# Optimization experiments

Hardware: AMD Instinct MI355X
Metric: run time of the kernel (lower is better)

The kernel has to match this reference:

```python
import jax, jax.numpy as jnp
import numpy as np
from jax import lax

N_LEVELS = 16
N_NODES = 65536  # nodes per level (= batch_size of trees at the root level)
FEATURES = 7
HIDDEN = 64


def setup_inputs() -> dict:
    key = jax.random.key(0)
    ks = jax.random.split(key, 11)
    contents = jax.random.normal(ks[0], (N_LEVELS, N_NODES, FEATURES), dtype=jnp.float32)
    children = jax.random.randint(ks[1], (N_LEVELS - 1, N_NODES, 2), 0, N_NODES, dtype=jnp.int32)
    s = 0.05
    return {
        'contents': contents,
        'children': children,
        'Wu': jax.random.normal(ks[2], (HIDDEN, FEATURES), dtype=jnp.float32) * s,
        'bu': jax.random.normal(ks[3], (HIDDEN,), dtype=jnp.float32) * s,
        'Wr': jax.random.normal(ks[4], (3 * HIDDEN, 3 * HIDDEN), dtype=jnp.float32) * s,
        'br': jax.random.normal(ks[5], (3 * HIDDEN,), dtype=jnp.float32) * s,
        'Wh': jax.random.normal(ks[6], (HIDDEN, 3 * HIDDEN), dtype=jnp.float32) * s,
        'bh': jax.random.normal(ks[7], (HIDDEN,), dtype=jnp.float32) * s,
        'Wz': jax.random.normal(ks[8], (4 * HIDDEN, 4 * HIDDEN), dtype=jnp.float32) * s,
        'bz': jax.random.normal(ks[9], (4 * HIDDEN,), dtype=jnp.float32) * s,
    }


def reference(contents, children, Wu, bu, Wr, br, Wh, bh, Wz, bz):
    h = Wu.shape[0]

    def leaf_embed(c):  # fc_u + relu
        return jax.nn.relu(c @ Wu.T + bu)

    # deepest level: all leaves -> up_embedding is just u_k
    up_top = leaf_embed(contents[-1])

    def step(up_next, xs):
        c, ch = xs                      # c: [N,F], ch: [N,2]
        u_k = leaf_embed(c)             # [N,h]
        h_L = up_next[ch[:, 0]]         # gather left children  [N,h]
        h_R = up_next[ch[:, 1]]         # gather right children [N,h]
        hhu = jnp.concatenate([h_L, h_R, u_k], axis=1)          # [N,3h]
        r = jax.nn.sigmoid(hhu @ Wr.T + br)                     # fc_r gate
        h_H = jax.nn.relu((r * hhu) @ Wh.T + bh)                # fc_h
        z = jnp.concatenate([h_H, hhu], axis=-1) @ Wz.T + bz    # [N,4h]
        # torch.stack([z_H,z_L,z_R,z_N],2) -> [N,h,4]; softmax over dim=1 (hidden)
        z = jnp.transpose(z.reshape(-1, 4, h), (0, 2, 1))       # [N,h,4]
        z = jax.nn.softmax(z, axis=1)
        h_new = z[:, :, 0] * h_H + z[:, :, 1] * h_L + z[:, :, 2] * h_R + z[:, :, 3] * u_k
        return h_new, None

    # process levels n-2, ..., 0 (bottom-up)
    xs = (contents[:-1][::-1], children[::-1])
    up0, _ = lax.scan(step, up_top, xs)
    # level 0 has batch_size roots -> h_out shape [batch_size, hidden]
    return up0
```

## Files before the change

### kernel.cpp

```cpp
#include <hip/hip_runtime.h>
#include <math.h>


#define N_NODES 65536
#define FEAT 7
#define H 64
#define MT 32
#define BLK 256

typedef __attribute__((ext_vector_type(8))) short bf16x8;
typedef __attribute__((ext_vector_type(4))) short short4v;
typedef __attribute__((ext_vector_type(4))) float f32x4;

__device__ __forceinline__ void split_bf16(float x, short& hi, short& lo) {
    unsigned u = __float_as_uint(x);
    unsigned r = (u + 0x7fffu + ((u >> 16) & 1u)) >> 16;
    hi = (short)r;
    float res = x - __uint_as_float(r << 16);
    unsigned u2 = __float_as_uint(res);
    unsigned r2 = (u2 + 0x7fffu + ((u2 >> 16) & 1u)) >> 16;
    lo = (short)r2;
}
__device__ __forceinline__ float bf2f(short h) {
    return __uint_as_float(((unsigned)(unsigned short)h) << 16);
}
__device__ __forceinline__ int zbidx(int row, int col) {
    return row * 192 + ((((col >> 3) ^ (row & 7)) << 3) | (col & 7));
}
__device__ __forceinline__ int zaidx(int row, int col) {
    return row * 64 + ((((col >> 3) ^ (row & 7)) << 3) | (col & 7));
}

#define MFMA3(acc, ah, al, bh8, bl8)                                              \
    acc = __builtin_amdgcn_mfma_f32_16x16x32_bf16(al, bh8, acc, 0, 0, 0);         \
    acc = __builtin_amdgcn_mfma_f32_16x16x32_bf16(ah, bl8, acc, 0, 0, 0);         \
    acc = __builtin_amdgcn_mfma_f32_16x16x32_bf16(ah, bh8, acc, 0, 0, 0);

__global__ __launch_bounds__(256) void grnn_prep(
    const float* __restrict__ Wr, const float* __restrict__ Wh,
    const float* __restrict__ Wz, short* __restrict__ wsp)
{
    int job = blockIdx.x * 4 + (threadIdx.x >> 6);
    int lane = threadIdx.x & 63;
    const float* src; int K, t, s; short* dst;
    short* ws_wh = wsp + 72 * 1024;
    short* ws_wz = wsp + 96 * 1024;
    if (job < 72)       { t = job / 6;            s = job % 6;        K = 192; src = Wr; dst = wsp   + job * 1024; }
    else if (job < 96)  { int j = job - 72; t = j / 6; s = j % 6;     K = 192; src = Wh; dst = ws_wh + j * 1024; }
    else                { int j = job - 96; t = j / 8; s = j % 8;     K = 256; src = Wz; dst = ws_wz + j * 1024; }
    int i  = t * 16 + (lane & 15);
    int k0 = s * 32 + (lane >> 4) * 8;
    const float* p = src + (size_t)i * K + k0;
    bf16x8 hi, lo;
#pragma unroll
    for (int e = 0; e < 8; ++e) { short h, l; split_bf16(p[e], h, l); hi[e] = h; lo[e] = l; }
    *(bf16x8*)(dst + lane * 8) = hi;
    *(bf16x8*)(dst + 512 + lane * 8) = lo;
}

__global__ __launch_bounds__(BLK) void grnn_leaf_kernel(
    const float* __restrict__ contents, const float* __restrict__ Wu,
    const float* __restrict__ bu, float* __restrict__ h_out)
{
    int t = blockIdx.x * BLK + threadIdx.x;
    int node = t >> 6;
    int j = t & 63;
    const float* c = contents + (size_t)15 * N_NODES * FEAT + (size_t)node * FEAT;
    float acc = bu[j];
#pragma unroll
    for (int f = 0; f < FEAT; ++f) acc += c[f] * Wu[j * FEAT + f];
    h_out[t] = fmaxf(acc, 0.f);
}

__global__ __launch_bounds__(BLK) void grnn_step_mfma(
    const float* __restrict__ contents_k, const int* __restrict__ children_k,
    const float* __restrict__ h_in,
    const float* __restrict__ Wu, const float* __restrict__ bu,
    const float* __restrict__ br, const float* __restrict__ bh,
    const float* __restrict__ bz,
    const short* __restrict__ wsp, float* __restrict__ h_out)
{
    __shared__ __align__(16) short zb_hi[MT * 192];
    __shared__ __align__(16) short zb_lo[MT * 192];
    __shared__ __align__(16) short ubuf[2][MT * 192];
    __shared__ __align__(16) float hacc[MT * 68];

    const int tid = threadIdx.x;
    const int node0 = blockIdx.x * MT;
    const int wv = tid >> 6, lane = tid & 63, lr = lane & 15, lh = lane >> 4;
    const short* wr_s = wsp;
    const short* wh_s = wsp + 72 * 1024;
    const short* wz_s = wsp + 96 * 1024;
    const f32x4 z4 = {0.f, 0.f, 0.f, 0.f};

    {
        int row = tid >> 2, q = tid & 3;
        int nd = row >> 1, side = row & 1;
        int child = children_k[(size_t)(node0 + nd) * 2 + side];
        const float4* src = (const float4*)(h_in + (size_t)child * H + q * 16);
#pragma unroll
        for (int f = 0; f < 4; ++f) {
            float4 v = src[f];
            float vv[4] = {v.x, v.y, v.z, v.w};
            int col0 = side * 64 + q * 16 + f * 4;
            int idx = zbidx(nd, col0);
            short4v h4, l4;
#pragma unroll
            for (int e = 0; e < 4; ++e) {
                short h, l; split_bf16(vv[e], h, l);
                h4[e] = h; l4[e] = l;
            }
            *(short4v*)&zb_hi[idx] = h4;
            *(short4v*)&zb_lo[idx] = l4;
        }
    }
    {
        int nd = tid >> 3, j0 = (tid & 7) * 8;
        float c[FEAT];
#pragma unroll
        for (int f = 0; f < FEAT; ++f) c[f] = contents_k[(size_t)(node0 + nd) * FEAT + f];
        bf16x8 hv, lv;
#pragma unroll
        for (int jj = 0; jj < 8; ++jj) {
            int j = j0 + jj;
            float a = bu[j];
#pragma unroll
            for (int f = 0; f < FEAT; ++f) a += c[f] * Wu[j * FEAT + f];
            a = fmaxf(a, 0.f);
            short h, l; split_bf16(a, h, l); hv[jj] = h; lv[jj] = l;
        }
        int idx = zbidx(nd, 128 + j0);
        *(bf16x8*)&zb_hi[idx] = hv;
        *(bf16x8*)&zb_lo[idx] = lv;
    }
    __syncthreads();

    f32x4 acc1[2][3];
#pragma unroll
    for (int mi = 0; mi < 2; ++mi)
#pragma unroll
        for (int ni = 0; ni < 3; ++ni) acc1[mi][ni] = z4;
    for (int s = 0; s < 6; ++s) {
        bf16x8 ah[2], al[2];
#pragma unroll
        for (int mi = 0; mi < 2; ++mi) {
            int idx = zbidx(mi * 16 + lr, s * 32 + lh * 8);
            ah[mi] = *(const bf16x8*)&zb_hi[idx];
            al[mi] = *(const bf16x8*)&zb_lo[idx];
        }
#pragma unroll
        for (int ni = 0; ni < 3; ++ni) {
            const short* bp = wr_s + ((3 * wv + ni) * 6 + s) * 1024;
            bf16x8 bh8 = *(const bf16x8*)(bp + lane * 8);
            bf16x8 bl8 = *(const bf16x8*)(bp + 512 + lane * 8);
#pragma unroll
            for (int mi = 0; mi < 2; ++mi) { MFMA3(acc1[mi][ni], ah[mi], al[mi], bh8, bl8); }
        }
    }
#pragma unroll
    for (int ni = 0; ni < 3; ++ni) {
        int i = (3 * wv + ni) * 16 + lr;
        float brv = br[i];
#pragma unroll
        for (int mi = 0; mi < 2; ++mi) {
#pragma unroll
            for (int r = 0; r < 4; ++r) {
                int nd = mi * 16 + lh * 4 + r;
                float v = acc1[mi][ni][r] + brv;
                float sg = 1.f / (1.f + __expf(-v));
                int xi = zbidx(nd, i);
                float x = bf2f(zb_hi[xi]) + bf2f(zb_lo[xi]);
                short h, l; split_bf16(sg * x, h, l);
                ubuf[0][xi] = h;
                ubuf[1][xi] = l;
            }
        }
    }
    __syncthreads();

    f32x4 acc2[2] = {z4, z4};
    for (int s = 0; s < 6; ++s) {
        bf16x8 ah[2], al[2];
#pragma unroll
        for (int mi = 0; mi < 2; ++mi) {
            int idx = zbidx(mi * 16 + lr, s * 32 + lh * 8);
            ah[mi] = *(const bf16x8*)&ubuf[0][idx];
            al[mi] = *(const bf16x8*)&ubuf[1][idx];
        }
        const short* bp = wh_s + (wv * 6 + s) * 1024;
        bf16x8 bh8 = *(const bf16x8*)(bp + lane * 8);
        bf16x8 bl8 = *(const bf16x8*)(bp + 512 + lane * 8);
#pragma unroll
        for (int mi = 0; mi < 2; ++mi) { MFMA3(acc2[mi], ah[mi], al[mi], bh8, bl8); }
    }
    __syncthreads();
    {
        int j = wv * 16 + lr;
        float bhv = bh[j];
#pragma unroll
        for (int mi = 0; mi < 2; ++mi) {
#pragma unroll
            for (int r = 0; r < 4; ++r) {
                int nd = mi * 16 + lh * 4 + r;
                float v = fmaxf(acc2[mi][r] + bhv, 0.f);
                short h, l; split_bf16(v, h, l);
                int idx = zaidx(nd, j);
                ubuf[0][idx] = h;
                ubuf[1][idx] = l;
            }
        }
    }
    __syncthreads();

    f32x4 acc3[2][4];
#pragma unroll
    for (int mi = 0; mi < 2; ++mi)
#pragma unroll
        for (int jh = 0; jh < 4; ++jh) acc3[mi][jh] = z4;
    for (int s = 0; s < 8; ++s) {
        bf16x8 ah[2], al[2];
#pragma unroll
        for (int mi = 0; mi < 2; ++mi) {
            int row = mi * 16 + lr;
            if (s < 2) {
                int idx = zaidx(row, s * 32 + lh * 8);
                ah[mi] = *(const bf16x8*)&ubuf[0][idx];
                al[mi] = *(const bf16x8*)&ubuf[1][idx];
            } else {
                int idx = zbidx(row, s * 32 + lh * 8 - 64);
                ah[mi] = *(const bf16x8*)&zb_hi[idx];
                al[mi] = *(const bf16x8*)&zb_lo[idx];
            }
        }
#pragma unroll
        for (int jh = 0; jh < 4; ++jh) {
            const short* bp = wz_s + ((wv * 4 + jh) * 8 + s) * 1024;
            bf16x8 bh8 = *(const bf16x8*)(bp + lane * 8);
            bf16x8 bl8 = *(const bf16x8*)(bp + 512 + lane * 8);
#pragma unroll
            for (int mi = 0; mi < 2; ++mi) { MFMA3(acc3[mi][jh], ah[mi], al[mi], bh8, bl8); }
        }
    }
    float bzv[4];
#pragma unroll
    for (int jh = 0; jh < 4; ++jh) bzv[jh] = bz[wv * 64 + jh * 16 + lr];
    float contrib[2][4][4];
#pragma unroll
    for (int mi = 0; mi < 2; ++mi) {
#pragma unroll
        for (int r = 0; r < 4; ++r) {
            float v0 = acc3[mi][0][r] + bzv[0];
            float v1 = acc3[mi][1][r] + bzv[1];
            float v2 = acc3[mi][2][r] + bzv[2];
            float v3 = acc3[mi][3][r] + bzv[3];
            float mx = fmaxf(fmaxf(v0, v1), fmaxf(v2, v3));
            mx = fmaxf(mx, __shfl_xor(mx, 1));
            mx = fmaxf(mx, __shfl_xor(mx, 2));
            mx = fmaxf(mx, __shfl_xor(mx, 4));
            mx = fmaxf(mx, __shfl_xor(mx, 8));
            float e0 = __expf(v0 - mx), e1 = __expf(v1 - mx);
            float e2 = __expf(v2 - mx), e3 = __expf(v3 - mx);
            float sm = e0 + e1 + e2 + e3;
            sm += __shfl_xor(sm, 1);
            sm += __shfl_xor(sm, 2);
            sm += __shfl_xor(sm, 4);
            sm += __shfl_xor(sm, 8);
            float inv = 1.f / sm;
            int nd = mi * 16 + lh * 4 + r;
            float e[4] = {e0, e1, e2, e3};
#pragma unroll
            for (int jh = 0; jh < 4; ++jh) {
                int n = wv * 64 + jh * 16 + lr;
                float comp;
                if (wv == 0) {
                    int idx = zaidx(nd, n);
                    comp = bf2f(ubuf[0][idx]) + bf2f(ubuf[1][idx]);
                } else {
                    int idx = zbidx(nd, n - 64);
                    comp = bf2f(zb_hi[idx]) + bf2f(zb_lo[idx]);
                }
                contrib[mi][jh][r] = e[jh] * inv * comp;
            }
        }
    }
    for (int p = 0; p < 4; ++p) {
        if (wv == p) {
#pragma unroll
            for (int mi = 0; mi < 2; ++mi)
#pragma unroll
                for (int r = 0; r < 4; ++r) {
                    int nd = mi * 16 + lh * 4 + r;
#pragma unroll
                    for (int jh = 0; jh < 4; ++jh) {
                        int hidx = nd * 68 + jh * 16 + lr;
                        if (p == 0) hacc[hidx] = contrib[mi][jh][r];
                        else        hacc[hidx] += contrib[mi][jh][r];
                    }
                }
        }
        __syncthreads();
    }
    for (int i = tid; i < MT * H; i += BLK) {
        int nd = i >> 6, j = i & 63;
        h_out[(size_t)(node0 + nd) * H + j] = hacc[nd * 68 + j];
    }
}

#define HP 196
#define HHP 68
#define ZP 260
#define NT1 16
__global__ __launch_bounds__(BLK) void grnn_step_v1(
    const float* __restrict__ contents_k, const int* __restrict__ children_k,
    const float* __restrict__ h_in,
    const float* __restrict__ Wu, const float* __restrict__ bu,
    const float* __restrict__ Wr, const float* __restrict__ br,
    const float* __restrict__ Wh, const float* __restrict__ bh,
    const float* __restrict__ Wz, const float* __restrict__ bz,
    float* __restrict__ h_out)
{
    __shared__ __align__(16) float hhu[NT1][HP];
    __shared__ __align__(16) float rh[NT1][HP];
    __shared__ __align__(16) float hH[NT1][HHP];
    __shared__ __align__(16) float zt[NT1][ZP];
    __shared__ float rden[NT1][4];
    const int tid = threadIdx.x;
    const int node0 = blockIdx.x * NT1;
    const int n = tid >> 4, c16 = tid & 15;
    {
        const float* cptr = contents_k + (size_t)(node0 + n) * FEAT;
        float cf[FEAT];
#pragma unroll
        for (int f = 0; f < FEAT; ++f) cf[f] = cptr[f];
#pragma unroll
        for (int jj = 0; jj < 4; ++jj) {
            int j = c16 + 16 * jj;
            float acc = bu[j];
#pragma unroll
            for (int f = 0; f < FEAT; ++f) acc += cf[f] * Wu[j * FEAT + f];
            hhu[n][128 + j] = fmaxf(acc, 0.f);
        }
#pragma unroll
        for (int it = 0; it < 8; ++it) {
            int t = tid + it * BLK;
            int nn = t >> 7, side = (t >> 6) & 1, j = t & 63;
            int child = children_k[(size_t)(node0 + nn) * 2 + side];
            hhu[nn][side * 64 + j] = h_in[(size_t)child * H + j];
        }
    }
    __syncthreads();
    {
        float acc[12];
#pragma unroll
        for (int ii = 0; ii < 12; ++ii) acc[ii] = br[c16 + 16 * ii];
        for (int k = 0; k < 192; k += 4) {
            float4 hv = *(const float4*)&hhu[n][k];
#pragma unroll
            for (int ii = 0; ii < 12; ++ii) {
                float4 w = *(const float4*)&Wr[(size_t)(c16 + 16 * ii) * 192 + k];
                acc[ii] += hv.x * w.x + hv.y * w.y + hv.z * w.z + hv.w * w.w;
            }
        }
#pragma unroll
        for (int ii = 0; ii < 12; ++ii) {
            int i = c16 + 16 * ii;
            rh[n][i] = (1.f / (1.f + __expf(-acc[ii]))) * hhu[n][i];
        }
    }
    __syncthreads();
    {
        float acc[4];
#pragma unroll
        for (int ii = 0; ii < 4; ++ii) acc[ii] = bh[c16 + 16 * ii];
        for (int k = 0; k < 192; k += 4) {
            float4 hv = *(const float4*)&rh[n][k];
#pragma unroll
            for (int ii = 0; ii < 4; ++ii) {
                float4 w = *(const float4*)&Wh[(size_t)(c16 + 16 * ii) * 192 + k];
                acc[ii] += hv.x * w.x + hv.y * w.y + hv.z * w.z + hv.w * w.w;
            }
        }
#pragma unroll
        for (int ii = 0; ii < 4; ++ii) hH[n][c16 + 16 * ii] = fmaxf(acc[ii], 0.f);
    }
    __syncthreads();
    {
        float acc[16];
#pragma unroll
        for (int ii = 0; ii < 16; ++ii) acc[ii] = bz[c16 + 16 * ii];
        for (int k = 0; k < 64; k += 4) {
            float4 hv = *(const float4*)&hH[n][k];
#pragma unroll
            for (int ii = 0; ii < 16; ++ii) {
                float4 w = *(const float4*)&Wz[(size_t)(c16 + 16 * ii) * 256 + k];
                acc[ii] += hv.x * w.x + hv.y * w.y + hv.z * w.z + hv.w * w.w;
            }
        }
        for (int k = 0; k < 192; k += 4) {
            float4 hv = *(const float4*)&hhu[n][k];
#pragma unroll
            for (int ii = 0; ii < 16; ++ii) {
                float4 w = *(const float4*)&Wz[(size_t)(c16 + 16 * ii) * 256 + 64 + k];
                acc[ii] += hv.x * w.x + hv.y * w.y + hv.z * w.z + hv.w * w.w;
            }
        }
#pragma unroll
        for (int ii = 0; ii < 16; ++ii) zt[n][c16 + 16 * ii] = acc[ii];
    }
    __syncthreads();
    {
        int sn = tid >> 4, g = (tid >> 2) & 3, q = tid & 3;
        float m = -INFINITY;
#pragma unroll
        for (int jj = 0; jj < 16; ++jj) m = fmaxf(m, zt[sn][g * 64 + q * 16 + jj]);
        m = fmaxf(m, __shfl_xor(m, 1));
        m = fmaxf(m, __shfl_xor(m, 2));
        float s = 0.f;
#pragma unroll
        for (int jj = 0; jj < 16; ++jj) {
            int idx = g * 64 + q * 16 + jj;
            float e = __expf(zt[sn][idx] - m);
            zt[sn][idx] = e;
            s += e;
        }
        s += __shfl_xor(s, 1);
        s += __shfl_xor(s, 2);
        if (q == 0) rden[sn][g] = 1.f / s;
    }
    __syncthreads();
    {
        size_t node = node0 + n;
#pragma unroll
        for (int jj = 0; jj < 4; ++jj) {
            int j = c16 + 16 * jj;
            float v = zt[n][j] * rden[n][0] * hH[n][j]
                    + zt[n][64 + j] * rden[n][1] * hhu[n][j]
                    + zt[n][128 + j] * rden[n][2] * hhu[n][64 + j]
                    + zt[n][192 + j] * rden[n][3] * hhu[n][128 + j];
            h_out[node * H + j] = v;
        }
    }
}

extern "C" void kernel_launch(void* const* d_in, const int* in_sizes, int n_in,
                              void* d_out, int out_size, void* d_ws, size_t ws_size,
                              hipStream_t stream) {
    const float* contents = (const float*)d_in[0];
    const int*   children = (const int*)d_in[1];
    const float* Wu = (const float*)d_in[2];
    const float* bu = (const float*)d_in[3];
    const float* Wr = (const float*)d_in[4];
    const float* br = (const float*)d_in[5];
    const float* Wh = (const float*)d_in[6];
    const float* bh = (const float*)d_in[7];
    const float* Wz = (const float*)d_in[8];
    const float* bz = (const float*)d_in[9];
    float* out = (float*)d_out;
    float* h_ws = (float*)d_ws;
    const size_t H_BYTES = (size_t)N_NODES * H * 4;
    const size_t W_BYTES = (72 + 24 + 128) * 2048;
    grnn_leaf_kernel<<<(N_NODES * H) / BLK, BLK, 0, stream>>>(contents, Wu, bu, h_ws);
    if (ws_size >= H_BYTES + W_BYTES) {
        short* wsp = (short*)((char*)d_ws + H_BYTES);
        grnn_prep<<<56, 256, 0, stream>>>(Wr, Wh, Wz, wsp);
        for (int k = 14; k >= 0; --k) {
            const float* hin = (((k + 1) & 1) == 0) ? out : h_ws;
            float* hout = ((k & 1) == 0) ? out : h_ws;
            grnn_step_mfma<<<N_NODES / MT, BLK, 0, stream>>>(
                contents + (size_t)k * N_NODES * FEAT,
                children + (size_t)k * N_NODES * 2,
                hin, Wu, bu, br, bh, bz, wsp, hout);
        }
    } else {
        for (int k = 14; k >= 0; --k) {
            const float* hin = (((k + 1) & 1) == 0) ? out : h_ws;
            float* hout = ((k & 1) == 0) ? out : h_ws;
            grnn_step_v1<<<N_NODES / NT1, BLK, 0, stream>>>(
                contents + (size_t)k * N_NODES * FEAT,
                children + (size_t)k * N_NODES * 2,
                hin, Wu, bu, Wr, br, Wh, bh, Wz, bz, hout);
        }
    }
}
```

Measured before the change: 1.295 ms.

## Store inter-level hidden state as split bf16 hi/lo and alias shared buffers

```diff
diff --git a/kernel.cpp b/kernel.cpp
--- a/kernel.cpp
+++ b/kernel.cpp
@@ -58,6 +58,22 @@
     *(bf16x8*)(dst + 512 + lane * 8) = lo;
 }
 
+__global__ __launch_bounds__(BLK) void grnn_leaf_bf(
+    const float* __restrict__ contents, const float* __restrict__ Wu,
+    const float* __restrict__ bu, short* __restrict__ hi_out, short* __restrict__ lo_out)
+{
+    int t = blockIdx.x * BLK + threadIdx.x;
+    int node = t >> 6;
+    int j = t & 63;
+    const float* c = contents + (size_t)15 * N_NODES * FEAT + (size_t)node * FEAT;
+    float acc = bu[j];
+#pragma unroll
+    for (int f = 0; f < FEAT; ++f) acc += c[f] * Wu[j * FEAT + f];
+    short h, l; split_bf16(fmaxf(acc, 0.f), h, l);
+    hi_out[t] = h;
+    lo_out[t] = l;
+}
+
 __global__ __launch_bounds__(BLK) void grnn_leaf_kernel(
     const float* __restrict__ contents, const float* __restrict__ Wu,
     const float* __restrict__ bu, float* __restrict__ h_out)
@@ -74,16 +90,20 @@
 
 __global__ __launch_bounds__(BLK) void grnn_step_mfma(
     const float* __restrict__ contents_k, const int* __restrict__ children_k,
-    const float* __restrict__ h_in,
+    const short* __restrict__ hin_hi, const short* __restrict__ hin_lo,
     const float* __restrict__ Wu, const float* __restrict__ bu,
     const float* __restrict__ br, const float* __restrict__ bh,
     const float* __restrict__ bz,
-    const short* __restrict__ wsp, float* __restrict__ h_out)
+    const short* __restrict__ wsp,
+    short* __restrict__ hout_hi, short* __restrict__ hout_lo,
+    float* __restrict__ out_f32, int is_final)
 {
-    __shared__ __align__(16) short zb_hi[MT * 192];
-    __shared__ __align__(16) short zb_lo[MT * 192];
-    __shared__ __align__(16) short ubuf[2][MT * 192];
-    __shared__ __align__(16) float hacc[MT * 68];
+    __shared__ __align__(16) short smem[4 * MT * 192];
+    short* zb_hi = smem;
+    short* zb_lo = smem + MT * 192;
+    short* ub0   = smem + 2 * MT * 192;
+    short* ub1   = smem + 3 * MT * 192;
+    float* hacc  = (float*)smem;
 
     const int tid = threadIdx.x;
     const int node0 = blockIdx.x * MT;
@@ -97,22 +117,15 @@
         int row = tid >> 2, q = tid & 3;
         int nd = row >> 1, side = row & 1;
         int child = children_k[(size_t)(node0 + nd) * 2 + side];
-        const float4* src = (const float4*)(h_in + (size_t)child * H + q * 16);
-#pragma unroll
-        for (int f = 0; f < 4; ++f) {
-            float4 v = src[f];
-            float vv[4] = {v.x, v.y, v.z, v.w};
-            int col0 = side * 64 + q * 16 + f * 4;
-            int idx = zbidx(nd, col0);
-            short4v h4, l4;
-#pragma unroll
-            for (int e = 0; e < 4; ++e) {
-                short h, l; split_bf16(vv[e], h, l);
-                h4[e] = h; l4[e] = l;
-            }
-            *(short4v*)&zb_hi[idx] = h4;
-            *(short4v*)&zb_lo[idx] = l4;
-        }
+        const bf16x8* srch = (const bf16x8*)(hin_hi + (size_t)child * H + q * 16);
+        const bf16x8* srcl = (const bf16x8*)(hin_lo + (size_t)child * H + q * 16);
+        int col0 = side * 64 + q * 16;
+        int i0 = zbidx(nd, col0);
+        int i1 = zbidx(nd, col0 + 8);
+        *(bf16x8*)&zb_hi[i0] = srch[0];
+        *(bf16x8*)&zb_hi[i1] = srch[1];
+        *(bf16x8*)&zb_lo[i0] = srcl[0];
+        *(bf16x8*)&zb_lo[i1] = srcl[1];
     }
     {
         int nd = tid >> 3, j0 = (tid & 7) * 8;
@@ -171,8 +184,8 @@
                 int xi = zbidx(nd, i);
                 float x = bf2f(zb_hi[xi]) + bf2f(zb_lo[xi]);
                 short h, l; split_bf16(sg * x, h, l);
-                ubuf[0][xi] = h;
-                ubuf[1][xi] = l;
+                ub0[xi] = h;
+                ub1[xi] = l;
             }
         }
     }
@@ -184,8 +197,8 @@
 #pragma unroll
         for (int mi = 0; mi < 2; ++mi) {
             int idx = zbidx(mi * 16 + lr, s * 32 + lh * 8);
-            ah[mi] = *(const bf16x8*)&ubuf[0][idx];
-            al[mi] = *(const bf16x8*)&ubuf[1][idx];
+            ah[mi] = *(const bf16x8*)&ub0[idx];
+            al[mi] = *(const bf16x8*)&ub1[idx];
         }
         const short* bp = wh_s + (wv * 6 + s) * 1024;
         bf16x8 bh8 = *(const bf16x8*)(bp + lane * 8);
@@ -205,8 +218,8 @@
                 float v = fmaxf(acc2[mi][r] + bhv, 0.f);
                 short h, l; split_bf16(v, h, l);
                 int idx = zaidx(nd, j);
-                ubuf[0][idx] = h;
-                ubuf[1][idx] = l;
+                ub0[idx] = h;
+                ub1[idx] = l;
             }
         }
     }
@@ -224,8 +237,8 @@
             int row = mi * 16 + lr;
             if (s < 2) {
                 int idx = zaidx(row, s * 32 + lh * 8);
-                ah[mi] = *(const bf16x8*)&ubuf[0][idx];
-                al[mi] = *(const bf16x8*)&ubuf[1][idx];
+                ah[mi] = *(const bf16x8*)&ub0[idx];
+                al[mi] = *(const bf16x8*)&ub1[idx];
             } else {
                 int idx = zbidx(row, s * 32 + lh * 8 - 64);
                 ah[mi] = *(const bf16x8*)&zb_hi[idx];
@@ -274,7 +287,7 @@
                 float comp;
                 if (wv == 0) {
                     int idx = zaidx(nd, n);
-                    comp = bf2f(ubuf[0][idx]) + bf2f(ubuf[1][idx]);
+                    comp = bf2f(ub0[idx]) + bf2f(ub1[idx]);
                 } else {
                     int idx = zbidx(nd, n - 64);
                     comp = bf2f(zb_hi[idx]) + bf2f(zb_lo[idx]);
@@ -283,6 +296,7 @@
             }
         }
     }
+    __syncthreads();
     for (int p = 0; p < 4; ++p) {
         if (wv == p) {
 #pragma unroll
@@ -300,9 +314,20 @@
         }
         __syncthreads();
     }
-    for (int i = tid; i < MT * H; i += BLK) {
-        int nd = i >> 6, j = i & 63;
-        h_out[(size_t)(node0 + nd) * H + j] = hacc[nd * 68 + j];
+    if (is_final) {
+        for (int i = tid; i < MT * H; i += BLK) {
+            int nd = i >> 6, j = i & 63;
+            out_f32[(size_t)(node0 + nd) * H + j] = hacc[nd * 68 + j];
+        }
+    } else {
+        for (int i = tid; i < MT * H; i += BLK) {
+            int nd = i >> 6, j = i & 63;
+            float v = hacc[nd * 68 + j];
+            short h, l; split_bf16(v, h, l);
+            size_t o = (size_t)(node0 + nd) * H + j;
+            hout_hi[o] = h;
+            hout_lo[o] = l;
+        }
     }
 }
 
@@ -456,22 +481,33 @@
     const float* Wz = (const float*)d_in[8];
     const float* bz = (const float*)d_in[9];
     float* out = (float*)d_out;
-    float* h_ws = (float*)d_ws;
-    const size_t H_BYTES = (size_t)N_NODES * H * 4;
+    const size_t HN = (size_t)N_NODES * H;
+    const size_t H_BYTES = HN * 4;
     const size_t W_BYTES = (72 + 24 + 128) * 2048;
-    grnn_leaf_kernel<<<(N_NODES * H) / BLK, BLK, 0, stream>>>(contents, Wu, bu, h_ws);
+
     if (ws_size >= H_BYTES + W_BYTES) {
-        short* wsp = (short*)((char*)d_ws + H_BYTES);
+        short* A_hi = (short*)d_ws;
+        short* A_lo = A_hi + HN;
+        short* B_hi = (short*)d_out;
+        short* B_lo = B_hi + HN;
+        short* wsp  = (short*)((char*)d_ws + H_BYTES);
+
         grnn_prep<<<56, 256, 0, stream>>>(Wr, Wh, Wz, wsp);
+        grnn_leaf_bf<<<(N_NODES * H) / BLK, BLK, 0, stream>>>(contents, Wu, bu, A_hi, A_lo);
         for (int k = 14; k >= 0; --k) {
-            const float* hin = (((k + 1) & 1) == 0) ? out : h_ws;
-            float* hout = ((k & 1) == 0) ? out : h_ws;
+            const short* in_hi = ((k + 1) & 1) ? A_hi : B_hi;
+            const short* in_lo = ((k + 1) & 1) ? A_lo : B_lo;
+            short* out_hi = (k & 1) ? A_hi : B_hi;
+            short* out_lo = (k & 1) ? A_lo : B_lo;
             grnn_step_mfma<<<N_NODES / MT, BLK, 0, stream>>>(
                 contents + (size_t)k * N_NODES * FEAT,
                 children + (size_t)k * N_NODES * 2,
-                hin, Wu, bu, br, bh, bz, wsp, hout);
+                in_hi, in_lo, Wu, bu, br, bh, bz, wsp,
+                out_hi, out_lo, out, (k == 0) ? 1 : 0);
         }
     } else {
+        float* h_ws = (float*)d_ws;
+        grnn_leaf_kernel<<<(N_NODES * H) / BLK, BLK, 0, stream>>>(contents, Wu, bu, h_ws);
         for (int k = 14; k >= 0; --k) {
             const float* hin = (((k + 1) & 1) == 0) ? out : h_ws;
             float* hout = ((k & 1) == 0) ? out : h_ws;
```

New measurement: 1.326 ms. +2.4%, slower.
